# Performance work log

Hardware: AMD Instinct MI355X
Metric: run time of the kernel (lower is better)

Reference implementation:

```python
import jax, jax.numpy as jnp
import numpy as np

B, S, D, H = 2, 2048, 1024, 16
DH = D // H


def setup_inputs() -> dict:
    key = jax.random.key(0)
    ks = jax.random.split(key, 13)
    s = 1.0 / np.sqrt(D)
    inp = {
        "q": jax.random.normal(ks[0], (B, S, D), jnp.float32),
        "k": jax.random.normal(ks[1], (B, S, D), jnp.float32),
        "v": jax.random.normal(ks[2], (B, S, D), jnp.float32),
        # causal mask [B,1,Q,K]: True = attend
        "attn_mask": jnp.broadcast_to(jnp.tril(jnp.ones((S, S), bool))[None, None], (B, 1, S, S)),
        "rel_bias": 0.1 * jax.random.normal(ks[3], (H, S, S), jnp.float32),
        "Wq": s * jax.random.normal(ks[4], (D, D), jnp.float32),
        "bq": jnp.zeros((D,), jnp.float32),
        "Wk": s * jax.random.normal(ks[5], (D, D), jnp.float32),
        "bk": jnp.zeros((D,), jnp.float32),
        "Wv": s * jax.random.normal(ks[6], (D, D), jnp.float32),
        "bv": jnp.zeros((D,), jnp.float32),
        "Wo": s * jax.random.normal(ks[7], (D, D), jnp.float32),
        "bo": jnp.zeros((D,), jnp.float32),
    }
    return inp


def reference(q, k, v, attn_mask, rel_bias, Wq, bq, Wk, bk, Wv, bv, Wo, bo):
    Bq, Q, Dm = q.shape
    K = k.shape[1]
    # projections -> [B, H, S, DH]
    qh = (q @ Wq + bq).reshape(Bq, Q, H, DH).transpose(0, 2, 1, 3)
    kh = (k @ Wk + bk).reshape(Bq, K, H, DH).transpose(0, 2, 1, 3)
    vh = (v @ Wv + bv).reshape(Bq, K, H, DH).transpose(0, 2, 1, 3)
    scores = jnp.einsum("bhqd,bhkd->bhqk", qh, kh) / np.sqrt(DH).astype(np.float32)
    scores = scores + rel_bias  # [H,Q,K] broadcasts over batch
    scores = jnp.where(attn_mask, scores, -jnp.inf)
    attn = jax.nn.softmax(scores, axis=-1)
    out = jnp.einsum("bhqk,bhkd->bhqd", attn, vh)
    out = out.transpose(0, 2, 1, 3).reshape(Bq, Q, Dm)
    return out @ Wo + bo
```

## Files before the change

kernel.cpp:

```cpp
#include <hip/hip_runtime.h>

typedef unsigned short u16;
typedef __attribute__((ext_vector_type(8))) short bf16x8;
typedef __attribute__((ext_vector_type(4))) float f32x4;
typedef __attribute__((ext_vector_type(4))) unsigned short us4;

#define B_ 2
#define S_ 2048
#define D_ 1024
#define H_ 16
#define DH_ 64
#define M_ 4096

__device__ __forceinline__ u16 f2bf(float f) {
  unsigned int u = __builtin_bit_cast(unsigned int, f);
  u += 0x7FFFu + ((u >> 16) & 1u);
  return (u16)(u >> 16);
}

__device__ __forceinline__ unsigned int cvtpk(float lo, float hi) {
  unsigned int r;
  asm("v_cvt_pk_bf16_f32 %0, %1, %2" : "=v"(r) : "v"(lo), "v"(hi));
  return r;
}

__device__ __forceinline__ float fexp2(float x) {
  float r;
  asm("v_exp_f32 %0, %1" : "=v"(r) : "v"(x));
  return r;
}

__device__ __forceinline__ void gload_lds16(const void* g, void* l) {
  __builtin_amdgcn_global_load_lds(
      (__attribute__((address_space(1))) void*)(g),
      (__attribute__((address_space(3))) void*)(l),
      16, 0, 0);
}

__global__ __launch_bounds__(256) void wprep_kernel(const float* __restrict__ W0,
                                                    const float* __restrict__ W1,
                                                    const float* __restrict__ W2,
                                                    const float* __restrict__ W3,
                                                    u16* __restrict__ Wt,
                                                    const float* __restrict__ qin,
                                                    const float* __restrict__ kin,
                                                    const float* __restrict__ vin,
                                                    u16* __restrict__ Xq,
                                                    u16* __restrict__ Xk,
                                                    u16* __restrict__ Xv) {
  int z = blockIdx.z;
  if (z < 4) {
    __shared__ float tile[32][33];
    const float* W = (z == 0) ? W0 : (z == 1) ? W1 : (z == 2) ? W2 : W3;
    u16* out = Wt + (size_t)z * D_ * D_;
    int tx = threadIdx.x, ty = threadIdx.y;
    int x = blockIdx.x * 32 + tx;
    for (int j = 0; j < 32; j += 8)
      tile[ty + j][tx] = W[(size_t)(blockIdx.y * 32 + ty + j) * D_ + x];
    __syncthreads();
    int x2 = blockIdx.y * 32 + tx;
    for (int j = 0; j < 32; j += 8)
      out[(size_t)(blockIdx.x * 32 + ty + j) * D_ + x2] = f2bf(tile[tx][ty + j]);
  } else {
    int zz = z - 4;
    const float* src = (zz == 0) ? qin : (zz == 1) ? kin : vin;
    u16* dst = (zz == 0) ? Xq : (zz == 1) ? Xk : Xv;
    int bid = blockIdx.y * 32 + blockIdx.x;
    int t = threadIdx.y * 32 + threadIdx.x;
    const float4* s4 = (const float4*)src;
    for (int i = 0; i < 4; ++i) {
      int idx = bid * 1024 + i * 256 + t;
      float4 v4 = s4[idx];
      us4 o;
      o[0] = f2bf(v4.x); o[1] = f2bf(v4.y); o[2] = f2bf(v4.z); o[3] = f2bf(v4.w);
      ((us4*)dst)[idx] = o;
    }
  }
}

__global__ __launch_bounds__(256) void gemm_qkv(const u16* __restrict__ Xq,
                                                const u16* __restrict__ Xk,
                                                const u16* __restrict__ Xv,
                                                const u16* __restrict__ Wt,
                                                const float* __restrict__ bq,
                                                const float* __restrict__ bk,
                                                const float* __restrict__ bv,
                                                u16* __restrict__ Qh,
                                                u16* __restrict__ Kh,
                                                u16* __restrict__ Vt) {
  __shared__ u16 As[128 * 64];
  __shared__ u16 Bs[128 * 64];
  int fid = blockIdx.x;
  int xcd = fid & 7, ii = fid >> 3;
  int grp = ii >> 3, yy = ii & 7;
  int gg = xcd * 12 + grp;
  int z = gg >> 5;
  int xx = gg & 31;
  const u16* A = (z == 0) ? Xq : (z == 1) ? Xk : Xv;
  const u16* Bt = Wt + (size_t)z * D_ * D_;
  const float* bias = (z == 0) ? bq : (z == 1) ? bk : bv;
  u16* O = (z == 0) ? Qh : (z == 1) ? Kh : Vt;

  int tid = threadIdx.x;
  int lane = tid & 63, wave = tid >> 6;
  int m0 = xx * 128, n0 = yy * 128;
  int wr = wave >> 1, wc = wave & 1;
  int fr = lane & 15, fk = (lane >> 4) * 8;

  f32x4 acc[4][4];
  const f32x4 vzero = {0.f, 0.f, 0.f, 0.f};
  for (int i = 0; i < 4; ++i)
    for (int j = 0; j < 4; ++j) acc[i][j] = vzero;

  for (int k0 = 0; k0 < D_; k0 += 64) {
    if (k0) __syncthreads();
    for (int i = 0; i < 4; ++i) {
      int base = ((i * 4 + wave) << 10);
      int ofs = base + lane * 16;
      int row = ofs >> 7;
      int scolb = (ofs & 127) ^ ((row & 7) << 4);
      gload_lds16(A + (size_t)(m0 + row) * D_ + k0 + (scolb >> 1), (char*)As + base);
      gload_lds16(Bt + (size_t)(n0 + row) * D_ + k0 + (scolb >> 1), (char*)Bs + base);
    }
    __syncthreads();
    for (int kh = 0; kh < 2; ++kh) {
      bf16x8 af[4], bfr[4];
      for (int mi = 0; mi < 4; ++mi) {
        int row = wr * 64 + mi * 16 + fr;
        af[mi] = *(const bf16x8*)((const char*)As + row * 128 +
                                  ((kh * 64 + fk * 2) ^ ((row & 7) << 4)));
      }
      for (int ni = 0; ni < 4; ++ni) {
        int row = wc * 64 + ni * 16 + fr;
        bfr[ni] = *(const bf16x8*)((const char*)Bs + row * 128 +
                                   ((kh * 64 + fk * 2) ^ ((row & 7) << 4)));
      }
      for (int mi = 0; mi < 4; ++mi)
        for (int ni = 0; ni < 4; ++ni)
          acc[mi][ni] =
              __builtin_amdgcn_mfma_f32_16x16x32_bf16(af[mi], bfr[ni], acc[mi][ni], 0, 0, 0);
    }
  }

  if (z == 2) {
    for (int mi = 0; mi < 4; ++mi) {
      int rowb = m0 + wr * 64 + mi * 16 + (lane >> 4) * 4;
      int bb2 = rowb >> 11, s0 = rowb & (S_ - 1);
      int l0 = s0 & 63;
      int p_local = ((l0 >> 5) & 1) * 32 + ((l0 >> 2) & 3) * 8 + ((l0 >> 4) & 1) * 4;
      int col2 = (s0 & ~63) | p_local;
      for (int ni = 0; ni < 4; ++ni) {
        int col = n0 + wc * 64 + ni * 16 + fr;
        int hh = col >> 6, dh = col & 63;
        float bv = bias[col];
        us4 pk;
        for (int r = 0; r < 4; ++r) pk[r] = f2bf(acc[mi][ni][r] + bv);
        *(us4*)(O + ((size_t)(bb2 * H_ + hh) * DH_ + dh) * S_ + col2) = pk;
      }
    }
  } else {
    float scale = (z == 0) ? 0.125f : 1.0f;
    for (int mi = 0; mi < 4; ++mi) {
      int rowb = m0 + wr * 64 + mi * 16 + (lane >> 4) * 4;
      for (int ni = 0; ni < 4; ++ni) {
        int col = n0 + wc * 64 + ni * 16 + fr;
        int hh = col >> 6, dh = col & 63;
        float bv = bias[col];
        for (int r = 0; r < 4; ++r) {
          int row = rowb + r;
          int bb2 = row >> 11, s = row & (S_ - 1);
          O[((size_t)(bb2 * H_ + hh) * S_ + s) * DH_ + dh] =
              f2bf((acc[mi][ni][r] + bv) * scale);
        }
      }
    }
  }
}

__global__ __launch_bounds__(256) void gemm_out(const u16* __restrict__ A,
                                                const u16* __restrict__ Bt,
                                                const float* __restrict__ bias,
                                                float* __restrict__ O) {
  __shared__ u16 As[64 * 64];
  __shared__ u16 Bs[128 * 64];
  int fid = blockIdx.x;
  int xcd = fid & 7, ii = fid >> 3;
  int grp = ii >> 3, yy = ii & 7;
  int gg = xcd * 8 + grp;
  int tid = threadIdx.x;
  int lane = tid & 63, wave = tid >> 6;
  int m0 = gg * 64, n0 = yy * 128;
  int fr = lane & 15, fk = (lane >> 4) * 8;

  f32x4 acc[4][2];
  const f32x4 vzero = {0.f, 0.f, 0.f, 0.f};
  for (int i = 0; i < 4; ++i)
    for (int j = 0; j < 2; ++j) acc[i][j] = vzero;

  for (int k0 = 0; k0 < D_; k0 += 64) {
    if (k0) __syncthreads();
    for (int i = 0; i < 2; ++i) {
      int base = ((i * 4 + wave) << 10);
      int ofs = base + lane * 16;
      int row = ofs >> 7;
      int scolb = (ofs & 127) ^ ((row & 7) << 4);
      gload_lds16(A + (size_t)(m0 + row) * D_ + k0 + (scolb >> 1), (char*)As + base);
    }
    for (int i = 0; i < 4; ++i) {
      int base = ((i * 4 + wave) << 10);
      int ofs = base + lane * 16;
      int row = ofs >> 7;
      int scolb = (ofs & 127) ^ ((row & 7) << 4);
      gload_lds16(Bt + (size_t)(n0 + row) * D_ + k0 + (scolb >> 1), (char*)Bs + base);
    }
    __syncthreads();
    for (int kh = 0; kh < 2; ++kh) {
      bf16x8 af[4], bfr[2];
      for (int mi = 0; mi < 4; ++mi) {
        int row = mi * 16 + fr;
        af[mi] = *(const bf16x8*)((const char*)As + row * 128 +
                                  ((kh * 64 + fk * 2) ^ ((row & 7) << 4)));
      }
      for (int ni = 0; ni < 2; ++ni) {
        int row = wave * 32 + ni * 16 + fr;
        bfr[ni] = *(const bf16x8*)((const char*)Bs + row * 128 +
                                   ((kh * 64 + fk * 2) ^ ((row & 7) << 4)));
      }
      for (int mi = 0; mi < 4; ++mi)
        for (int ni = 0; ni < 2; ++ni)
          acc[mi][ni] =
              __builtin_amdgcn_mfma_f32_16x16x32_bf16(af[mi], bfr[ni], acc[mi][ni], 0, 0, 0);
    }
  }

  for (int mi = 0; mi < 4; ++mi) {
    int rowb = m0 + mi * 16 + (lane >> 4) * 4;
    for (int ni = 0; ni < 2; ++ni) {
      int col = n0 + wave * 32 + ni * 16 + fr;
      float bv = bias[col];
      for (int r = 0; r < 4; ++r)
        O[(size_t)(rowb + r) * D_ + col] = acc[mi][ni][r] + bv;
    }
  }
}

__global__ __launch_bounds__(256, 4) void attn_kernel(const u16* __restrict__ Qh,
                                                      const u16* __restrict__ Kh,
                                                      const u16* __restrict__ Vt,
                                                      const float* __restrict__ relb,
                                                      u16* __restrict__ attnout) {
  __shared__ u16 KVs[2][2][4096];

  int fid = blockIdx.x;
  int rr = fid >> 8, c = fid & 255;
  int j = c >> 3, e = c & 7;
  int s = (rr & 1) ? j : 31 - j;
  int h = (rr & 1) ? e + 8 : e;
  int b = rr >> 1;

  int w = threadIdx.x >> 6, lane = threadIdx.x & 63;
  int fr = lane & 15, g = lane >> 4;
  int q0w = s * 64 + w * 16;
  int qme = q0w + fr;
  int bh = b * H_ + h;
  int sx = (fr & 7) << 4;

  int kind = w >> 1;
  int i0 = (w & 1) * 4;
  int srow_lo = lane >> 3;
  int scb = (lane & 7) * 16;

  const u16* Qb = Qh + ((size_t)bh * S_ + q0w) * DH_;
  bf16x8 qf0 = *(const bf16x8*)(Qb + fr * DH_ + 8 * g);
  bf16x8 qf1 = *(const bf16x8*)(Qb + fr * DH_ + 32 + 8 * g);

  const float* Bq = relb + (size_t)h * S_ * S_ + (size_t)qme * S_ + 4 * g;
  const float LOG2E = 1.44269504f;

  int T = s + 1;

  auto STAGE = [&](int buf, int kb) {
    for (int i = 0; i < 4; ++i) {
      int ii = i0 + i;
      int row = ii * 8 + srow_lo;
      int cbs = scb ^ ((row & 7) << 4);
      const u16* src;
      if (kind == 0)
        src = Kh + ((size_t)bh * S_ + kb + row) * DH_ + (cbs >> 1);
      else
        src = Vt + ((size_t)bh * DH_ + row) * S_ + kb + (cbs >> 1);
      gload_lds16(src, &KVs[kind][buf][ii * 512]);
    }
  };

  f32x4 acc[4];
  const f32x4 vzero = {0.f, 0.f, 0.f, 0.f};
  for (int f4 = 0; f4 < 4; ++f4) acc[f4] = vzero;
  float m = -1.0e4f, l = 0.f;

  STAGE(0, 0);
  f32x4 bi[4], bn[4];
  for (int cc = 0; cc < 4; ++cc) bi[cc] = *(const f32x4*)(Bq + 16 * cc);
  __syncthreads();

  for (int t = 0; t < T; ++t) {
    int kb = t * 64;
    int buf = t & 1;
    bool diag = (t == T - 1);
    if (!diag) {
      STAGE(buf ^ 1, kb + 64);
      for (int cc = 0; cc < 4; ++cc) bn[cc] = *(const f32x4*)(Bq + kb + 64 + 16 * cc);
    }

    const u16* Kt = &KVs[0][buf][0];
    const u16* Vl = &KVs[1][buf][0];

    f32x4 sc[4];
    __builtin_amdgcn_s_setprio(1);
    for (int cc = 0; cc < 4; ++cc) {
      bf16x8 k0 = *(const bf16x8*)(Kt + (16 * cc + fr) * 64 + (((16 * g) ^ sx) >> 1));
      bf16x8 k1 = *(const bf16x8*)(Kt + (16 * cc + fr) * 64 + (((64 + 16 * g) ^ sx) >> 1));
      f32x4 z = __builtin_amdgcn_mfma_f32_16x16x32_bf16(k0, qf0, bi[cc], 0, 0, 0);
      z = __builtin_amdgcn_mfma_f32_16x16x32_bf16(k1, qf1, z, 0, 0, 0);
      sc[cc] = z;
    }
    __builtin_amdgcn_s_setprio(0);
    if (diag) {
      for (int cc = 0; cc < 4; ++cc)
        for (int r = 0; r < 4; ++r) {
          int key = kb + 16 * cc + 4 * g + r;
          sc[cc][r] = (key <= qme) ? sc[cc][r] : -1e30f;
        }
    }
    float pm = sc[0][0];
    for (int cc = 0; cc < 4; ++cc)
      for (int r = 0; r < 4; ++r) pm = fmaxf(pm, sc[cc][r]);
    pm = fmaxf(pm, __shfl_xor(pm, 16));
    pm = fmaxf(pm, __shfl_xor(pm, 32));
    if (!__all(pm - m <= 8.0f)) {
      float mn = fmaxf(m, pm);
      float corr = __expf(m - mn);
      m = mn;
      l *= corr;
      float c0 = __shfl(corr, 4 * g + 0);
      float c1 = __shfl(corr, 4 * g + 1);
      float c2 = __shfl(corr, 4 * g + 2);
      float c3 = __shfl(corr, 4 * g + 3);
      for (int f4 = 0; f4 < 4; ++f4) {
        acc[f4][0] *= c0; acc[f4][1] *= c1; acc[f4][2] *= c2; acc[f4][3] *= c3;
      }
    }
    float nms = m * -LOG2E;
    float rs = 0.f;
    for (int cc = 0; cc < 4; ++cc)
      for (int r = 0; r < 4; ++r) {
        sc[cc][r] = fexp2(fmaf(sc[cc][r], LOG2E, nms));
        rs += sc[cc][r];
      }
    l += rs;
    union { unsigned int w4[4]; bf16x8 v; } pp[2];
    for (int jj = 0; jj < 2; ++jj) {
      pp[jj].w4[0] = cvtpk(sc[2 * jj][0], sc[2 * jj][1]);
      pp[jj].w4[1] = cvtpk(sc[2 * jj][2], sc[2 * jj][3]);
      pp[jj].w4[2] = cvtpk(sc[2 * jj + 1][0], sc[2 * jj + 1][1]);
      pp[jj].w4[3] = cvtpk(sc[2 * jj + 1][2], sc[2 * jj + 1][3]);
    }
    __builtin_amdgcn_s_setprio(1);
    for (int f4 = 0; f4 < 4; ++f4) {
      for (int jj = 0; jj < 2; ++jj) {
        bf16x8 vv = *(const bf16x8*)(Vl + (f4 * 16 + fr) * 64 +
                                     (((jj * 64 + g * 16) ^ sx) >> 1));
        acc[f4] = __builtin_amdgcn_mfma_f32_16x16x32_bf16(pp[jj].v, vv, acc[f4], 0, 0, 0);
      }
    }
    __builtin_amdgcn_s_setprio(0);
    for (int cc = 0; cc < 4; ++cc) bi[cc] = bn[cc];
    __syncthreads();
  }

  l += __shfl_xor(l, 16);
  l += __shfl_xor(l, 32);
  float il = 1.f / l;
  for (int r = 0; r < 4; ++r) {
    float ilr = __shfl(il, 4 * g + r);
    int qq = q0w + 4 * g + r;
    u16* ob = attnout + ((size_t)b * S_ + qq) * D_ + h * 64;
    for (int f4 = 0; f4 < 4; ++f4) ob[f4 * 16 + fr] = f2bf(acc[f4][r] * ilr);
  }
}

extern "C" void kernel_launch(void* const* d_in, const int* in_sizes, int n_in,
                              void* d_out, int out_size, void* d_ws, size_t ws_size,
                              hipStream_t stream) {
  const float* q = (const float*)d_in[0];
  const float* k = (const float*)d_in[1];
  const float* v = (const float*)d_in[2];
  const float* rb = (const float*)d_in[4];
  const float* Wq = (const float*)d_in[5];
  const float* bq = (const float*)d_in[6];
  const float* Wk = (const float*)d_in[7];
  const float* bk = (const float*)d_in[8];
  const float* Wv = (const float*)d_in[9];
  const float* bv = (const float*)d_in[10];
  const float* Wo = (const float*)d_in[11];
  const float* bo = (const float*)d_in[12];
  float* out = (float*)d_out;

  char* ws = (char*)d_ws;
  const size_t SZ = (size_t)M_ * D_ * 2;
  u16* Xq = (u16*)(ws);
  u16* Xk = (u16*)(ws + SZ);
  u16* Xv = (u16*)(ws + 2 * SZ);
  u16* Qh = (u16*)(ws + 3 * SZ);
  u16* Kh = (u16*)(ws + 4 * SZ);
  u16* Vt = (u16*)(ws + 5 * SZ);
  u16* Wt = (u16*)(ws + 6 * SZ);
  u16* Xb = Xq;

  wprep_kernel<<<dim3(32, 32, 7), dim3(32, 8), 0, stream>>>(Wq, Wk, Wv, Wo, Wt,
                                                            q, k, v, Xq, Xk, Xv);

  gemm_qkv<<<dim3(768), 256, 0, stream>>>(Xq, Xk, Xv, Wt, bq, bk, bv, Qh, Kh, Vt);

  attn_kernel<<<dim3(1024), 256, 0, stream>>>(Qh, Kh, Vt, rb, Xb);

  gemm_out<<<dim3(512), 256, 0, stream>>>(Xb, Wt + 3 * (size_t)D_ * D_, bo, out);
}
```

Before: 128.8 us.

## Process 128 queries per attention block to reuse staged K/V tiles

Each wave now handles two 16-row query groups (A and B), so a block covers 128 query rows instead of 64 and the grid halves to 512 blocks. Every K/V tile staged into LDS and every LDS fragment load feeds twice as many MFMAs, cutting K/V global traffic and LDS reads per unit of work. The block-to-tile mapping is reordered to pair heads and batches, and launch bounds drop to 3 blocks per CU to allow the extra accumulators and registers. The cost is more register pressure, lower occupancy, fewer blocks for load balancing under causal masking, and masking applied on the last two diagonal tiles.

Result: slower. 142.4 us (+10.6%).

```diff
diff --git a/kernel.cpp b/kernel.cpp
--- a/kernel.cpp
+++ b/kernel.cpp
@@ -244,7 +244,7 @@
   }
 }
 
-__global__ __launch_bounds__(256, 4) void attn_kernel(const u16* __restrict__ Qh,
+__global__ __launch_bounds__(256, 3) void attn_kernel(const u16* __restrict__ Qh,
                                                       const u16* __restrict__ Kh,
                                                       const u16* __restrict__ Vt,
                                                       const float* __restrict__ relb,
@@ -252,16 +252,17 @@
   __shared__ u16 KVs[2][2][4096];
 
   int fid = blockIdx.x;
-  int rr = fid >> 8, c = fid & 255;
-  int j = c >> 3, e = c & 7;
-  int s = (rr & 1) ? j : 31 - j;
-  int h = (rr & 1) ? e + 8 : e;
-  int b = rr >> 1;
+  int r = fid >> 8, c = fid & 255;
+  int e = c & 7, g2 = c >> 3;
+  int h = e + 8 * (g2 & 1);
+  int b = (g2 >> 1) & 1;
+  int p = g2 >> 2;
+  int s128 = r ? p : 15 - p;
 
   int w = threadIdx.x >> 6, lane = threadIdx.x & 63;
   int fr = lane & 15, g = lane >> 4;
-  int q0w = s * 64 + w * 16;
-  int qme = q0w + fr;
+  int q0w = s128 * 128 + w * 32;
+  int qmeA = q0w + fr, qmeB = q0w + 16 + fr;
   int bh = b * H_ + h;
   int sx = (fr & 7) << 4;
 
@@ -271,13 +272,16 @@
   int scb = (lane & 7) * 16;
 
   const u16* Qb = Qh + ((size_t)bh * S_ + q0w) * DH_;
-  bf16x8 qf0 = *(const bf16x8*)(Qb + fr * DH_ + 8 * g);
-  bf16x8 qf1 = *(const bf16x8*)(Qb + fr * DH_ + 32 + 8 * g);
-
-  const float* Bq = relb + (size_t)h * S_ * S_ + (size_t)qme * S_ + 4 * g;
+  bf16x8 qA0 = *(const bf16x8*)(Qb + fr * DH_ + 8 * g);
+  bf16x8 qA1 = *(const bf16x8*)(Qb + fr * DH_ + 32 + 8 * g);
+  bf16x8 qB0 = *(const bf16x8*)(Qb + (16 + fr) * DH_ + 8 * g);
+  bf16x8 qB1 = *(const bf16x8*)(Qb + (16 + fr) * DH_ + 32 + 8 * g);
+
+  const float* BqA = relb + (size_t)h * S_ * S_ + (size_t)qmeA * S_ + 4 * g;
+  const float* BqB = relb + (size_t)h * S_ * S_ + (size_t)qmeB * S_ + 4 * g;
   const float LOG2E = 1.44269504f;
 
-  int T = s + 1;
+  int T = 2 * s128 + 2;
 
   auto STAGE = [&](int buf, int kb) {
     for (int i = 0; i < 4; ++i) {
@@ -293,99 +297,147 @@
     }
   };
 
-  f32x4 acc[4];
+  f32x4 accA[4], accB[4];
   const f32x4 vzero = {0.f, 0.f, 0.f, 0.f};
-  for (int f4 = 0; f4 < 4; ++f4) acc[f4] = vzero;
-  float m = -1.0e4f, l = 0.f;
+  for (int f4 = 0; f4 < 4; ++f4) { accA[f4] = vzero; accB[f4] = vzero; }
+  float mA = -1.0e4f, lA = 0.f, mB = -1.0e4f, lB = 0.f;
 
   STAGE(0, 0);
-  f32x4 bi[4], bn[4];
-  for (int cc = 0; cc < 4; ++cc) bi[cc] = *(const f32x4*)(Bq + 16 * cc);
+  f32x4 biA[4], biB[4], bnA[4], bnB[4];
+  for (int cc = 0; cc < 4; ++cc) {
+    biA[cc] = *(const f32x4*)(BqA + 16 * cc);
+    biB[cc] = *(const f32x4*)(BqB + 16 * cc);
+  }
   __syncthreads();
 
   for (int t = 0; t < T; ++t) {
     int kb = t * 64;
     int buf = t & 1;
-    bool diag = (t == T - 1);
-    if (!diag) {
+    if (t + 1 < T) {
       STAGE(buf ^ 1, kb + 64);
-      for (int cc = 0; cc < 4; ++cc) bn[cc] = *(const f32x4*)(Bq + kb + 64 + 16 * cc);
+      for (int cc = 0; cc < 4; ++cc) {
+        bnA[cc] = *(const f32x4*)(BqA + kb + 64 + 16 * cc);
+        bnB[cc] = *(const f32x4*)(BqB + kb + 64 + 16 * cc);
+      }
     }
 
     const u16* Kt = &KVs[0][buf][0];
     const u16* Vl = &KVs[1][buf][0];
 
-    f32x4 sc[4];
+    f32x4 sA[4], sB[4];
     __builtin_amdgcn_s_setprio(1);
     for (int cc = 0; cc < 4; ++cc) {
       bf16x8 k0 = *(const bf16x8*)(Kt + (16 * cc + fr) * 64 + (((16 * g) ^ sx) >> 1));
       bf16x8 k1 = *(const bf16x8*)(Kt + (16 * cc + fr) * 64 + (((64 + 16 * g) ^ sx) >> 1));
-      f32x4 z = __builtin_amdgcn_mfma_f32_16x16x32_bf16(k0, qf0, bi[cc], 0, 0, 0);
-      z = __builtin_amdgcn_mfma_f32_16x16x32_bf16(k1, qf1, z, 0, 0, 0);
-      sc[cc] = z;
+      f32x4 zA = __builtin_amdgcn_mfma_f32_16x16x32_bf16(k0, qA0, biA[cc], 0, 0, 0);
+      sA[cc] = __builtin_amdgcn_mfma_f32_16x16x32_bf16(k1, qA1, zA, 0, 0, 0);
+      f32x4 zB = __builtin_amdgcn_mfma_f32_16x16x32_bf16(k0, qB0, biB[cc], 0, 0, 0);
+      sB[cc] = __builtin_amdgcn_mfma_f32_16x16x32_bf16(k1, qB1, zB, 0, 0, 0);
     }
     __builtin_amdgcn_s_setprio(0);
-    if (diag) {
+    if (t >= 2 * s128) {
       for (int cc = 0; cc < 4; ++cc)
-        for (int r = 0; r < 4; ++r) {
-          int key = kb + 16 * cc + 4 * g + r;
-          sc[cc][r] = (key <= qme) ? sc[cc][r] : -1e30f;
-        }
-    }
-    float pm = sc[0][0];
-    for (int cc = 0; cc < 4; ++cc)
-      for (int r = 0; r < 4; ++r) pm = fmaxf(pm, sc[cc][r]);
-    pm = fmaxf(pm, __shfl_xor(pm, 16));
-    pm = fmaxf(pm, __shfl_xor(pm, 32));
-    if (!__all(pm - m <= 8.0f)) {
-      float mn = fmaxf(m, pm);
-      float corr = __expf(m - mn);
-      m = mn;
-      l *= corr;
-      float c0 = __shfl(corr, 4 * g + 0);
-      float c1 = __shfl(corr, 4 * g + 1);
-      float c2 = __shfl(corr, 4 * g + 2);
-      float c3 = __shfl(corr, 4 * g + 3);
-      for (int f4 = 0; f4 < 4; ++f4) {
-        acc[f4][0] *= c0; acc[f4][1] *= c1; acc[f4][2] *= c2; acc[f4][3] *= c3;
-      }
-    }
-    float nms = m * -LOG2E;
-    float rs = 0.f;
-    for (int cc = 0; cc < 4; ++cc)
-      for (int r = 0; r < 4; ++r) {
-        sc[cc][r] = fexp2(fmaf(sc[cc][r], LOG2E, nms));
-        rs += sc[cc][r];
-      }
-    l += rs;
-    union { unsigned int w4[4]; bf16x8 v; } pp[2];
+        for (int rr = 0; rr < 4; ++rr) {
+          int key = kb + 16 * cc + 4 * g + rr;
+          sA[cc][rr] = (key <= qmeA) ? sA[cc][rr] : -1e30f;
+          sB[cc][rr] = (key <= qmeB) ? sB[cc][rr] : -1e30f;
+        }
+    }
+    {
+      float pm = sA[0][0];
+      for (int cc = 0; cc < 4; ++cc)
+        for (int rr = 0; rr < 4; ++rr) pm = fmaxf(pm, sA[cc][rr]);
+      pm = fmaxf(pm, __shfl_xor(pm, 16));
+      pm = fmaxf(pm, __shfl_xor(pm, 32));
+      if (!__all(pm - mA <= 8.0f)) {
+        float mn = fmaxf(mA, pm);
+        float corr = __expf(mA - mn);
+        mA = mn;
+        lA *= corr;
+        float c0 = __shfl(corr, 4 * g + 0);
+        float c1 = __shfl(corr, 4 * g + 1);
+        float c2 = __shfl(corr, 4 * g + 2);
+        float c3 = __shfl(corr, 4 * g + 3);
+        for (int f4 = 0; f4 < 4; ++f4) {
+          accA[f4][0] *= c0; accA[f4][1] *= c1; accA[f4][2] *= c2; accA[f4][3] *= c3;
+        }
+      }
+      float nms = mA * -LOG2E, rs = 0.f;
+      for (int cc = 0; cc < 4; ++cc)
+        for (int rr = 0; rr < 4; ++rr) {
+          sA[cc][rr] = fexp2(fmaf(sA[cc][rr], LOG2E, nms));
+          rs += sA[cc][rr];
+        }
+      lA += rs;
+    }
+    {
+      float pm = sB[0][0];
+      for (int cc = 0; cc < 4; ++cc)
+        for (int rr = 0; rr < 4; ++rr) pm = fmaxf(pm, sB[cc][rr]);
+      pm = fmaxf(pm, __shfl_xor(pm, 16));
+      pm = fmaxf(pm, __shfl_xor(pm, 32));
+      if (!__all(pm - mB <= 8.0f)) {
+        float mn = fmaxf(mB, pm);
+        float corr = __expf(mB - mn);
+        mB = mn;
+        lB *= corr;
+        float c0 = __shfl(corr, 4 * g + 0);
+        float c1 = __shfl(corr, 4 * g + 1);
+        float c2 = __shfl(corr, 4 * g + 2);
+        float c3 = __shfl(corr, 4 * g + 3);
+        for (int f4 = 0; f4 < 4; ++f4) {
+          accB[f4][0] *= c0; accB[f4][1] *= c1; accB[f4][2] *= c2; accB[f4][3] *= c3;
+        }
+      }
+      float nms = mB * -LOG2E, rs = 0.f;
+      for (int cc = 0; cc < 4; ++cc)
+        for (int rr = 0; rr < 4; ++rr) {
+          sB[cc][rr] = fexp2(fmaf(sB[cc][rr], LOG2E, nms));
+          rs += sB[cc][rr];
+        }
+      lB += rs;
+    }
+    union { unsigned int w4[4]; bf16x8 v; } ppA[2], ppB[2];
     for (int jj = 0; jj < 2; ++jj) {
-      pp[jj].w4[0] = cvtpk(sc[2 * jj][0], sc[2 * jj][1]);
-      pp[jj].w4[1] = cvtpk(sc[2 * jj][2], sc[2 * jj][3]);
-      pp[jj].w4[2] = cvtpk(sc[2 * jj + 1][0], sc[2 * jj + 1][1]);
-      pp[jj].w4[3] = cvtpk(sc[2 * jj + 1][2], sc[2 * jj + 1][3]);
+      ppA[jj].w4[0] = cvtpk(sA[2 * jj][0], sA[2 * jj][1]);
+      ppA[jj].w4[1] = cvtpk(sA[2 * jj][2], sA[2 * jj][3]);
+      ppA[jj].w4[2] = cvtpk(sA[2 * jj + 1][0], sA[2 * jj + 1][1]);
+      ppA[jj].w4[3] = cvtpk(sA[2 * jj + 1][2], sA[2 * jj + 1][3]);
+      ppB[jj].w4[0] = cvtpk(sB[2 * jj][0], sB[2 * jj][1]);
+      ppB[jj].w4[1] = cvtpk(sB[2 * jj][2], sB[2 * jj][3]);
+      ppB[jj].w4[2] = cvtpk(sB[2 * jj + 1][0], sB[2 * jj + 1][1]);
+      ppB[jj].w4[3] = cvtpk(sB[2 * jj + 1][2], sB[2 * jj + 1][3]);
     }
     __builtin_amdgcn_s_setprio(1);
     for (int f4 = 0; f4 < 4; ++f4) {
       for (int jj = 0; jj < 2; ++jj) {
         bf16x8 vv = *(const bf16x8*)(Vl + (f4 * 16 + fr) * 64 +
                                      (((jj * 64 + g * 16) ^ sx) >> 1));
-        acc[f4] = __builtin_amdgcn_mfma_f32_16x16x32_bf16(pp[jj].v, vv, acc[f4], 0, 0, 0);
+        accA[f4] = __builtin_amdgcn_mfma_f32_16x16x32_bf16(ppA[jj].v, vv, accA[f4], 0, 0, 0);
+        accB[f4] = __builtin_amdgcn_mfma_f32_16x16x32_bf16(ppB[jj].v, vv, accB[f4], 0, 0, 0);
       }
     }
     __builtin_amdgcn_s_setprio(0);
-    for (int cc = 0; cc < 4; ++cc) bi[cc] = bn[cc];
+    for (int cc = 0; cc < 4; ++cc) { biA[cc] = bnA[cc]; biB[cc] = bnB[cc]; }
     __syncthreads();
   }
 
-  l += __shfl_xor(l, 16);
-  l += __shfl_xor(l, 32);
-  float il = 1.f / l;
-  for (int r = 0; r < 4; ++r) {
-    float ilr = __shfl(il, 4 * g + r);
-    int qq = q0w + 4 * g + r;
-    u16* ob = attnout + ((size_t)b * S_ + qq) * D_ + h * 64;
-    for (int f4 = 0; f4 < 4; ++f4) ob[f4 * 16 + fr] = f2bf(acc[f4][r] * ilr);
+  lA += __shfl_xor(lA, 16);
+  lA += __shfl_xor(lA, 32);
+  lB += __shfl_xor(lB, 16);
+  lB += __shfl_xor(lB, 32);
+  float ilA = 1.f / lA, ilB = 1.f / lB;
+  for (int rr = 0; rr < 4; ++rr) {
+    float ia = __shfl(ilA, 4 * g + rr);
+    float ib = __shfl(ilB, 4 * g + rr);
+    int qqA = q0w + 4 * g + rr;
+    int qqB = q0w + 16 + 4 * g + rr;
+    u16* obA = attnout + ((size_t)b * S_ + qqA) * D_ + h * 64;
+    u16* obB = attnout + ((size_t)b * S_ + qqB) * D_ + h * 64;
+    for (int f4 = 0; f4 < 4; ++f4) {
+      obA[f4 * 16 + fr] = f2bf(accA[f4][rr] * ia);
+      obB[f4 * 16 + fr] = f2bf(accB[f4][rr] * ib);
+    }
   }
 }
 
@@ -422,7 +474,7 @@
 
   gemm_qkv<<<dim3(768), 256, 0, stream>>>(Xq, Xk, Xv, Wt, bq, bk, bv, Qh, Kh, Vt);
 
-  attn_kernel<<<dim3(1024), 256, 0, stream>>>(Qh, Kh, Vt, rb, Xb);
+  attn_kernel<<<dim3(512), 256, 0, stream>>>(Qh, Kh, Vt, rb, Xb);
 
   gemm_out<<<dim3(512), 256, 0, stream>>>(Xb, Wt + 3 * (size_t)D_ * D_, bo, out);
 }
```
